# Optimization experiments

Measured on AMD Instinct MI355X. Metric: run time of the kernel, lower is better.

## Reference

```python
import jax, jax.numpy as jnp
import numpy as np

N = 50000      # nodes
E = 600000     # edges
F_IN = 128     # num_features
H = 128        # hidden_dim

def setup_inputs() -> dict:
    key = jax.random.key(0)
    k1, k2, k3 = jax.random.split(key, 3)
    x = jax.random.normal(k1, (N, F_IN), dtype=jnp.float32)
    W = jax.random.normal(k2, (F_IN, H), dtype=jnp.float32) * 0.05
    b = jnp.zeros((H,), dtype=jnp.float32)
    edge_index = jax.random.randint(k3, (2, E), 0, N, dtype=jnp.int64)
    return {"x": x, "W": W, "b": b, "edge_index": edge_index}

def reference(x, W, b, edge_index):
    # GCNConv (PyG default): add self-loops, symmetric deg^-1/2 normalization,
    # out[t] = sum_{(s,t) in E'} norm(s,t) * (x @ W)[s] + b, then relu.
    n = x.shape[0]
    loops = jnp.arange(n, dtype=edge_index.dtype)
    src = jnp.concatenate([edge_index[0], loops])  # [E+N]
    dst = jnp.concatenate([edge_index[1], loops])  # [E+N]
    xw = x @ W                                      # [N, H]
    deg = jax.ops.segment_sum(jnp.ones_like(dst, dtype=xw.dtype), dst,
                              num_segments=n)       # [N], >=1 due to self-loops
    dinv = jax.lax.rsqrt(deg)
    norm = dinv[src] * dinv[dst]                    # [E+N]
    msg = xw[src] * norm[:, None]                   # [E+N, H] gather
    agg = jax.ops.segment_sum(msg, dst, num_segments=n)  # [N, H] scatter-add
    out = jax.nn.relu(agg + b)
    # F.dropout(training=False) is identity in eval mode.
    return out
```

## Files before the change

kernel.cpp:

```cpp
#include <hip/hip_runtime.h>
#include <stdint.h>


#define FDIM 128
#define HDIM 128
#define SCAN_CHUNK 1024

using s8v   = __attribute__((ext_vector_type(8))) short;
using f32x4 = __attribute__((ext_vector_type(4))) float;

__device__ __forceinline__ unsigned bf16rn(float f) {
    unsigned u = __float_as_uint(f);
    return (u + 0x7fffu + ((u >> 16) & 1u)) >> 16;
}
__device__ __forceinline__ void upfma(unsigned w, float ds, float& lo, float& hi) {
    lo = fmaf(ds, __uint_as_float(w << 16), lo);
    hi = fmaf(ds, __uint_as_float(w & 0xffff0000u), hi);
}

__global__ __launch_bounds__(256) void k_setup(int* __restrict__ deg,
                                               const float* __restrict__ W,
                                               uint4* __restrict__ Warr,
                                               int n, int packW) {
    const int i = blockIdx.x * 256 + threadIdx.x;
    if (i < n) deg[i] = 0;
    if (packW && i < (FDIM / 8) * HDIM) {
        const int chunk = i >> 7, nn = i & 127;
        float v[8];
#pragma unroll
        for (int j = 0; j < 8; ++j) v[j] = W[(chunk * 8 + j) * HDIM + nn];
        uint4 o;
        o.x = bf16rn(v[0]) | (bf16rn(v[1]) << 16);
        o.y = bf16rn(v[2]) | (bf16rn(v[3]) << 16);
        o.z = bf16rn(v[4]) | (bf16rn(v[5]) << 16);
        o.w = bf16rn(v[6]) | (bf16rn(v[7]) << 16);
        Warr[i] = o;
    }
}

__global__ __launch_bounds__(256) void k_count_xcast(const int* __restrict__ dst,
                                                     int* __restrict__ deg,
                                                     int* __restrict__ slot,
                                                     const float* __restrict__ x,
                                                     uint4* __restrict__ xb,
                                                     int e, int n, int fillBlocks) {
    if ((int)blockIdx.x < fillBlocks) {
        const int i = blockIdx.x * 256 + threadIdx.x;
        if (i < e) slot[i] = atomicAdd(&deg[dst[i]], 1);
    } else if (xb) {
        const long long idx = (long long)(blockIdx.x - fillBlocks) * 256 + threadIdx.x;
        if (idx >= (long long)n * (FDIM / 8)) return;
        const float4* xp = (const float4*)x + idx * 2;
        const float4 a = xp[0], b = xp[1];
        uint4 o;
        o.x = bf16rn(a.x) | (bf16rn(a.y) << 16);
        o.y = bf16rn(a.z) | (bf16rn(a.w) << 16);
        o.z = bf16rn(b.x) | (bf16rn(b.y) << 16);
        o.w = bf16rn(b.z) | (bf16rn(b.w) << 16);
        xb[idx] = o;
    }
}

__global__ __launch_bounds__(256) void k_scan1(const int* __restrict__ deg,
                                               int* __restrict__ rowptr,
                                               int* __restrict__ partials,
                                               float* __restrict__ dinv, int n) {
    __shared__ int sdata[256];
    const int tid = threadIdx.x;
    const int base = blockIdx.x * SCAN_CHUNK + tid * 4;
    int v[4];
    int s = 0;
#pragma unroll
    for (int j = 0; j < 4; ++j) {
        int idx = base + j;
        v[j] = (idx < n) ? deg[idx] : 0;
        if (idx < n) dinv[idx] = rsqrtf((float)v[j] + 1.0f);
        s += v[j];
    }
    sdata[tid] = s;
    __syncthreads();
    for (int off = 1; off < 256; off <<= 1) {
        int t = (tid >= off) ? sdata[tid - off] : 0;
        __syncthreads();
        sdata[tid] += t;
        __syncthreads();
    }
    int run = sdata[tid] - s;
#pragma unroll
    for (int j = 0; j < 4; ++j) {
        int idx = base + j;
        if (idx < n) rowptr[idx] = run;
        run += v[j];
    }
    if (tid == 255) {
        partials[blockIdx.x] = sdata[255];
        if (blockIdx.x == (int)gridDim.x - 1) rowptr[n] = sdata[255];
    }
}

__global__ __launch_bounds__(64) void k_scan2(int* __restrict__ partials, int nb) {
    int l = threadIdx.x;
    int v = (l < nb) ? partials[l] : 0;
    int inc = v;
    for (int off = 1; off < 64; off <<= 1) {
        int t = __shfl_up(inc, off);
        if (l >= off) inc += t;
    }
    if (l < nb) partials[l] = inc - v;
}

__global__ __launch_bounds__(256) void k_fill(const int* __restrict__ src,
                                              const int* __restrict__ dst,
                                              const int* __restrict__ slot,
                                              const int* __restrict__ rowptr,
                                              const int* __restrict__ partials,
                                              int* __restrict__ elist, int e, int nb) {
    __shared__ int coffs[64];
    const int tid = threadIdx.x;
    if (tid < 64) {
        int v = (tid < nb) ? partials[tid] : 0;
        int inc = v;
        for (int off = 1; off < 64; off <<= 1) {
            int t = __shfl_up(inc, off);
            if (tid >= off) inc += t;
        }
        coffs[tid] = inc - v;
    }
    __syncthreads();
    const int i = blockIdx.x * 256 + tid;
    if (i < e) {
        const int d = dst[i];
        elist[rowptr[d] + coffs[d >> 10] + slot[i]] = src[i];
    }
}

__global__ __launch_bounds__(256) void k_gather_gemm(
    const uint4* __restrict__ xb, const float* __restrict__ dinv,
    const int* __restrict__ rowptr, const int* __restrict__ partials,
    const int* __restrict__ elist, const uint4* __restrict__ Warr,
    const float* __restrict__ bias, float* __restrict__ out, int n, int nb) {
    __shared__ uint4 zlds[16][16];
    __shared__ int coffs[64];
    const int tid = threadIdx.x;
    const int r = tid >> 4, q = tid & 15;
    const int node = blockIdx.x * 16 + r;
    const int wave = tid >> 6, lane = tid & 63;
    const int l16 = lane & 15, lg = lane >> 4;

    if (tid < 64) {
        int v = (tid < nb) ? partials[tid] : 0;
        int inc = v;
        for (int off = 1; off < 64; off <<= 1) {
            int t = __shfl_up(inc, off);
            if (tid >= off) inc += t;
        }
        coffs[tid] = inc - v;
    }
    __syncthreads();

    int beg = 0, end = 0;
    float di = 0.0f;
    if (node < n) {
        beg = rowptr[node] + coffs[node >> 10];
        end = rowptr[node + 1] + coffs[(node + 1) >> 10];
        di = dinv[node];
    }

    s8v wf[2][4];
#pragma unroll
    for (int ntl = 0; ntl < 2; ++ntl)
#pragma unroll
        for (int ks = 0; ks < 4; ++ks)
            wf[ntl][ks] = *(const s8v*)&Warr[(ks * 4 + lg) * 128 +
                                             (wave * 2 + ntl) * 16 + l16];
    const float bv0 = bias[(wave * 2 + 0) * 16 + l16];
    const float bv1 = bias[(wave * 2 + 1) * 16 + l16];

    if (node < n) {
        const uint4* xq = xb + q;
        float a0 = 0.f, a1 = 0.f, a2 = 0.f, a3 = 0.f,
              a4 = 0.f, a5 = 0.f, a6 = 0.f, a7 = 0.f;
        {
            const uint4 v = xq[(size_t)node * 16];
            upfma(v.x, di, a0, a1); upfma(v.y, di, a2, a3);
            upfma(v.z, di, a4, a5); upfma(v.w, di, a6, a7);
        }
        if (beg < end) {
            const int last = end - 1;
            int sidx[4];
#pragma unroll
            for (int k = 0; k < 4; ++k) {
                const int jj = beg + k;
                sidx[k] = elist[jj < end ? jj : last];
            }
            for (int j = beg; j < end; j += 4) {
                int snext[4];
#pragma unroll
                for (int k = 0; k < 4; ++k) {
                    const int jj = j + 4 + k;
                    snext[k] = elist[jj < end ? jj : last];
                }
                float dw[4];
                uint4 u[4];
#pragma unroll
                for (int k = 0; k < 4; ++k) {
                    dw[k] = (j + k < end) ? dinv[sidx[k]] : 0.0f;
                    u[k] = xq[(size_t)sidx[k] * 16];
                }
#pragma unroll
                for (int k = 0; k < 4; ++k) {
                    upfma(u[k].x, dw[k], a0, a1); upfma(u[k].y, dw[k], a2, a3);
                    upfma(u[k].z, dw[k], a4, a5); upfma(u[k].w, dw[k], a6, a7);
                }
#pragma unroll
                for (int k = 0; k < 4; ++k) sidx[k] = snext[k];
            }
        }
        uint4 o;
        o.x = bf16rn(a0 * di) | (bf16rn(a1 * di) << 16);
        o.y = bf16rn(a2 * di) | (bf16rn(a3 * di) << 16);
        o.z = bf16rn(a4 * di) | (bf16rn(a5 * di) << 16);
        o.w = bf16rn(a6 * di) | (bf16rn(a7 * di) << 16);
        zlds[r][q ^ r] = o;
    }
    __syncthreads();

    s8v afr[4];
#pragma unroll
    for (int ks = 0; ks < 4; ++ks)
        afr[ks] = *(const s8v*)&zlds[l16][(ks * 4 + lg) ^ l16];

#pragma unroll
    for (int ntl = 0; ntl < 2; ++ntl) {
        f32x4 acc = (f32x4){0.f, 0.f, 0.f, 0.f};
#pragma unroll
        for (int ks = 0; ks < 4; ++ks)
            acc = __builtin_amdgcn_mfma_f32_16x16x32_bf16(afr[ks], wf[ntl][ks], acc, 0, 0, 0);
        const int col = (wave * 2 + ntl) * 16 + l16;
        const float bv = ntl ? bv1 : bv0;
#pragma unroll
        for (int rr = 0; rr < 4; ++rr) {
            const int row = blockIdx.x * 16 + lg * 4 + rr;
            if (row < n)
                __builtin_nontemporal_store(fmaxf(acc[rr] + bv, 0.0f),
                                            &out[(size_t)row * HDIM + col]);
        }
    }
}

__global__ __launch_bounds__(256) void k_fill_fb(const int* __restrict__ src,
                                                 const int* __restrict__ dst,
                                                 const int* __restrict__ slot,
                                                 const int* __restrict__ rowptr,
                                                 const int* __restrict__ coff,
                                                 int* __restrict__ elist, int e) {
    int i = blockIdx.x * 256 + threadIdx.x;
    if (i < e) {
        const int d = dst[i];
        elist[rowptr[d] + coff[d >> 10] + slot[i]] = src[i];
    }
}

__global__ __launch_bounds__(256) void k_gather_f32(const float* __restrict__ x,
                                                    const float* __restrict__ dinv,
                                                    const int* __restrict__ rowptr,
                                                    const int* __restrict__ coff,
                                                    const int* __restrict__ elist,
                                                    float* __restrict__ z, int n) {
    const int lane = threadIdx.x & 31;
    const int node = blockIdx.x * 8 + (threadIdx.x >> 5);
    if (node >= n) return;
    const float di = dinv[node];
    float4 v = ((const float4*)(x + (size_t)node * FDIM))[lane];
    float4 sum;
    sum.x = di * v.x; sum.y = di * v.y; sum.z = di * v.z; sum.w = di * v.w;
    const int beg = rowptr[node] + coff[node >> 10];
    const int end = rowptr[node + 1] + coff[(node + 1) >> 10];
    for (int j = beg; j < end; ++j) {
        const int s = elist[j];
        const float ds = dinv[s];
        const float4 u = ((const float4*)(x + (size_t)s * FDIM))[lane];
        sum.x = fmaf(ds, u.x, sum.x);
        sum.y = fmaf(ds, u.y, sum.y);
        sum.z = fmaf(ds, u.z, sum.z);
        sum.w = fmaf(ds, u.w, sum.w);
    }
    float4 o;
    o.x = di * sum.x; o.y = di * sum.y; o.z = di * sum.z; o.w = di * sum.w;
    ((float4*)(z + (size_t)node * FDIM))[lane] = o;
}

__global__ __launch_bounds__(512) void k_gemm_relu(const float* __restrict__ W,
                                                   const float* __restrict__ bias,
                                                   float* __restrict__ zo, int n) {
    __shared__ float Wl[FDIM * HDIM];
    __shared__ float xs[4][FDIM];
    const int t = threadIdx.x;
    const int h = t & (HDIM - 1);
    const int g = t >> 7;
    {
        const float4* W4 = (const float4*)W;
        float4* Wl4 = (float4*)Wl;
        for (int i = t; i < FDIM * HDIM / 4; i += 512) Wl4[i] = W4[i];
    }
    __syncthreads();
    const float bv = bias[h];
    const int nq = (n + 3) >> 2;
    for (int q = blockIdx.x; q < nq; q += gridDim.x) {
        const int row = q * 4 + g;
        if (row < n) xs[g][h] = zo[(size_t)row * HDIM + h];
        __syncthreads();
        if (row < n) {
            float acc = bv;
#pragma unroll
            for (int k = 0; k < FDIM; ++k)
                acc = fmaf(xs[g][k], Wl[k * HDIM + h], acc);
            zo[(size_t)row * HDIM + h] = fmaxf(acc, 0.0f);
        }
        __syncthreads();
    }
}

extern "C" void kernel_launch(void* const* d_in, const int* in_sizes, int n_in,
                              void* d_out, int out_size, void* d_ws, size_t ws_size,
                              hipStream_t stream) {
    const float* x = (const float*)d_in[0];
    const float* W = (const float*)d_in[1];
    const float* b = (const float*)d_in[2];
    const int* ei = (const int*)d_in[3];
    float* out = (float*)d_out;

    const int H = in_sizes[2];
    const int F = in_sizes[1] / H;
    const int N = in_sizes[0] / F;
    const int E = in_sizes[3] / 2;
    const int* srcp = ei;
    const int* dstp = ei + E;

    auto align256 = [](size_t v) { return (v + 255) & ~(size_t)255; };
    char* ws = (char*)d_ws;
    size_t off = 0;
    int* deg = (int*)(ws + off);      off += align256((size_t)N * 4);
    float* dinv = (float*)(ws + off); off += align256((size_t)N * 4);
    int* rowptr = (int*)(ws + off);   off += align256((size_t)(N + 1) * 4);
    int* slot = (int*)(ws + off);     off += align256((size_t)E * 4);
    int* partials = (int*)(ws + off); off += 256;
    int* elist = (int*)(ws + off);    off += align256((size_t)E * 4);
    uint4* xb = (uint4*)(ws + off);   off += align256((size_t)N * FDIM * 2);
    uint4* Warr = (uint4*)(ws + off); off += align256((size_t)(FDIM / 8) * HDIM * 16);
    const bool fast = (ws_size >= off) && (N <= 64 * SCAN_CHUNK);

    const int nblk_scan = (N + SCAN_CHUNK - 1) / SCAN_CHUNK;
    const int fillBlocks = (E + 255) / 256;

    k_setup<<<(N + 255) / 256, 256, 0, stream>>>(deg, W, fast ? Warr : nullptr,
                                                 N, fast ? 1 : 0);
    if (fast) {
        const long long nchunks = (long long)N * (FDIM / 8);
        const int castBlocks = (int)((nchunks + 255) / 256);
        k_count_xcast<<<fillBlocks + castBlocks, 256, 0, stream>>>(
            dstp, deg, slot, x, xb, E, N, fillBlocks);
        k_scan1<<<nblk_scan, 256, 0, stream>>>(deg, rowptr, partials, dinv, N);
        k_fill<<<fillBlocks, 256, 0, stream>>>(srcp, dstp, slot, rowptr, partials,
                                               elist, E, nblk_scan);
        k_gather_gemm<<<(N + 15) / 16, 256, 0, stream>>>(xb, dinv, rowptr, partials,
                                                         elist, Warr, b, out, N,
                                                         nblk_scan);
    } else {
        k_count_xcast<<<fillBlocks, 256, 0, stream>>>(dstp, deg, slot, x, nullptr,
                                                      E, N, fillBlocks);
        k_scan1<<<nblk_scan, 256, 0, stream>>>(deg, rowptr, partials, dinv, N);
        k_scan2<<<1, 64, 0, stream>>>(partials, nblk_scan);
        k_fill_fb<<<fillBlocks, 256, 0, stream>>>(srcp, dstp, slot, rowptr, partials,
                                                  elist, E);
        k_gather_f32<<<(N + 7) / 8, 256, 0, stream>>>(x, dinv, rowptr, partials,
                                                      elist, out, N);
        k_gemm_relu<<<512, 512, 0, stream>>>(W, b, out, N);
    }
}
```

Before: 85.28 us.

## Move x/W bf16 casts into scan kernel, split atomic degree count

The bf16 casts of x and W move out of the degree-count kernel and the setup kernel into the block scan kernel as extra blocks. The count kernel is now standalone and each thread handles two edges. The aim is to keep the atomic-heavy count pass short and lightweight, and to hide the cast work alongside the small scan launch. The cast traffic now runs after the count instead of overlapping with it, which could serialise work that was concurrent before.

```diff
diff --git a/kernel.cpp b/kernel.cpp
--- a/kernel.cpp
+++ b/kernel.cpp
@@ -18,14 +18,77 @@
     hi = fmaf(ds, __uint_as_float(w & 0xffff0000u), hi);
 }
 
-__global__ __launch_bounds__(256) void k_setup(int* __restrict__ deg,
-                                               const float* __restrict__ W,
-                                               uint4* __restrict__ Warr,
-                                               int n, int packW) {
+__global__ __launch_bounds__(256) void k_setup(int* __restrict__ deg, int n) {
     const int i = blockIdx.x * 256 + threadIdx.x;
     if (i < n) deg[i] = 0;
-    if (packW && i < (FDIM / 8) * HDIM) {
-        const int chunk = i >> 7, nn = i & 127;
+}
+
+__global__ __launch_bounds__(256) void k_count(const int* __restrict__ dst,
+                                               int* __restrict__ deg,
+                                               int* __restrict__ slot, int e) {
+    const int i = blockIdx.x * 512 + threadIdx.x;
+    if (i < e) slot[i] = atomicAdd(&deg[dst[i]], 1);
+    const int j = i + 256;
+    if (j < e) slot[j] = atomicAdd(&deg[dst[j]], 1);
+}
+
+__global__ __launch_bounds__(256) void k_scanaux(const int* __restrict__ deg,
+                                                 int* __restrict__ rowptr,
+                                                 int* __restrict__ partials,
+                                                 float* __restrict__ dinv,
+                                                 const float* __restrict__ x,
+                                                 uint4* __restrict__ xb,
+                                                 const float* __restrict__ W,
+                                                 uint4* __restrict__ Warr,
+                                                 int n, int nblk, int castBlocks) {
+    const int b = blockIdx.x;
+    const int tid = threadIdx.x;
+    if (b < nblk) {
+        __shared__ int sdata[256];
+        const int base = b * SCAN_CHUNK + tid * 4;
+        int v[4];
+        int s = 0;
+#pragma unroll
+        for (int j = 0; j < 4; ++j) {
+            int idx = base + j;
+            v[j] = (idx < n) ? deg[idx] : 0;
+            if (idx < n) dinv[idx] = rsqrtf((float)v[j] + 1.0f);
+            s += v[j];
+        }
+        sdata[tid] = s;
+        __syncthreads();
+        for (int off = 1; off < 256; off <<= 1) {
+            int t = (tid >= off) ? sdata[tid - off] : 0;
+            __syncthreads();
+            sdata[tid] += t;
+            __syncthreads();
+        }
+        int run = sdata[tid] - s;
+#pragma unroll
+        for (int j = 0; j < 4; ++j) {
+            int idx = base + j;
+            if (idx < n) rowptr[idx] = run;
+            run += v[j];
+        }
+        if (tid == 255) {
+            partials[b] = sdata[255];
+            if (b == nblk - 1) rowptr[n] = sdata[255];
+        }
+    } else if (b < nblk + castBlocks) {
+        const long long idx = (long long)(b - nblk) * 256 + tid;
+        if (idx >= (long long)n * (FDIM / 8)) return;
+        const float4* xp = (const float4*)x + idx * 2;
+        const float4 a = xp[0], c = xp[1];
+        uint4 o;
+        o.x = bf16rn(a.x) | (bf16rn(a.y) << 16);
+        o.y = bf16rn(a.z) | (bf16rn(a.w) << 16);
+        o.z = bf16rn(c.x) | (bf16rn(c.y) << 16);
+        o.w = bf16rn(c.z) | (bf16rn(c.w) << 16);
+        xb[idx] = o;
+    } else {
+        const int t = (b - nblk - castBlocks) * 256 + tid;
+        if (t >= (FDIM / 8) * HDIM) return;
+        const int chunk = t >> 7, nn = t & 127;
         float v[8];
 #pragma unroll
         for (int j = 0; j < 8; ++j) v[j] = W[(chunk * 8 + j) * HDIM + nn];
@@ -34,67 +97,7 @@
         o.y = bf16rn(v[2]) | (bf16rn(v[3]) << 16);
         o.z = bf16rn(v[4]) | (bf16rn(v[5]) << 16);
         o.w = bf16rn(v[6]) | (bf16rn(v[7]) << 16);
-        Warr[i] = o;
-    }
-}
-
-__global__ __launch_bounds__(256) void k_count_xcast(const int* __restrict__ dst,
-                                                     int* __restrict__ deg,
-                                                     int* __restrict__ slot,
-                                                     const float* __restrict__ x,
-                                                     uint4* __restrict__ xb,
-                                                     int e, int n, int fillBlocks) {
-    if ((int)blockIdx.x < fillBlocks) {
-        const int i = blockIdx.x * 256 + threadIdx.x;
-        if (i < e) slot[i] = atomicAdd(&deg[dst[i]], 1);
-    } else if (xb) {
-        const long long idx = (long long)(blockIdx.x - fillBlocks) * 256 + threadIdx.x;
-        if (idx >= (long long)n * (FDIM / 8)) return;
-        const float4* xp = (const float4*)x + idx * 2;
-        const float4 a = xp[0], b = xp[1];
-        uint4 o;
-        o.x = bf16rn(a.x) | (bf16rn(a.y) << 16);
-        o.y = bf16rn(a.z) | (bf16rn(a.w) << 16);
-        o.z = bf16rn(b.x) | (bf16rn(b.y) << 16);
-        o.w = bf16rn(b.z) | (bf16rn(b.w) << 16);
-        xb[idx] = o;
-    }
-}
-
-__global__ __launch_bounds__(256) void k_scan1(const int* __restrict__ deg,
-                                               int* __restrict__ rowptr,
-                                               int* __restrict__ partials,
-                                               float* __restrict__ dinv, int n) {
-    __shared__ int sdata[256];
-    const int tid = threadIdx.x;
-    const int base = blockIdx.x * SCAN_CHUNK + tid * 4;
-    int v[4];
-    int s = 0;
-#pragma unroll
-    for (int j = 0; j < 4; ++j) {
-        int idx = base + j;
-        v[j] = (idx < n) ? deg[idx] : 0;
-        if (idx < n) dinv[idx] = rsqrtf((float)v[j] + 1.0f);
-        s += v[j];
-    }
-    sdata[tid] = s;
-    __syncthreads();
-    for (int off = 1; off < 256; off <<= 1) {
-        int t = (tid >= off) ? sdata[tid - off] : 0;
-        __syncthreads();
-        sdata[tid] += t;
-        __syncthreads();
-    }
-    int run = sdata[tid] - s;
-#pragma unroll
-    for (int j = 0; j < 4; ++j) {
-        int idx = base + j;
-        if (idx < n) rowptr[idx] = run;
-        run += v[j];
-    }
-    if (tid == 255) {
-        partials[blockIdx.x] = sdata[255];
-        if (blockIdx.x == (int)gridDim.x - 1) rowptr[n] = sdata[255];
+        Warr[t] = o;
     }
 }
 
@@ -352,24 +355,25 @@
 
     const int nblk_scan = (N + SCAN_CHUNK - 1) / SCAN_CHUNK;
     const int fillBlocks = (E + 255) / 256;
-
-    k_setup<<<(N + 255) / 256, 256, 0, stream>>>(deg, W, fast ? Warr : nullptr,
-                                                 N, fast ? 1 : 0);
+    const int countBlocks = (E + 511) / 512;
+
+    k_setup<<<(N + 255) / 256, 256, 0, stream>>>(deg, N);
+    k_count<<<countBlocks, 256, 0, stream>>>(dstp, deg, slot, E);
     if (fast) {
         const long long nchunks = (long long)N * (FDIM / 8);
         const int castBlocks = (int)((nchunks + 255) / 256);
-        k_count_xcast<<<fillBlocks + castBlocks, 256, 0, stream>>>(
-            dstp, deg, slot, x, xb, E, N, fillBlocks);
-        k_scan1<<<nblk_scan, 256, 0, stream>>>(deg, rowptr, partials, dinv, N);
+        const int warrBlocks = ((FDIM / 8) * HDIM + 255) / 256;
+        k_scanaux<<<nblk_scan + castBlocks + warrBlocks, 256, 0, stream>>>(
+            deg, rowptr, partials, dinv, x, xb, W, Warr, N, nblk_scan, castBlocks);
         k_fill<<<fillBlocks, 256, 0, stream>>>(srcp, dstp, slot, rowptr, partials,
                                                elist, E, nblk_scan);
         k_gather_gemm<<<(N + 15) / 16, 256, 0, stream>>>(xb, dinv, rowptr, partials,
                                                          elist, Warr, b, out, N,
                                                          nblk_scan);
     } else {
-        k_count_xcast<<<fillBlocks, 256, 0, stream>>>(dstp, deg, slot, x, nullptr,
-                                                      E, N, fillBlocks);
-        k_scan1<<<nblk_scan, 256, 0, stream>>>(deg, rowptr, partials, dinv, N);
+        k_scanaux<<<nblk_scan, 256, 0, stream>>>(deg, rowptr, partials, dinv,
+                                                 x, nullptr, W, nullptr,
+                                                 N, nblk_scan, 0);
         k_scan2<<<1, 64, 0, stream>>>(partials, nblk_scan);
         k_fill_fb<<<fillBlocks, 256, 0, stream>>>(srcp, dstp, slot, rowptr, partials,
                                                   elist, E);
```

Measured after the change: 85.96 us. No clear change (+0.8%).
